# Kernel tuning notes

Measured on AMD Instinct MI355X. Metric: run time of the kernel, lower is better.

## Reference

```python
import jax, jax.numpy as jnp
import numpy as np

D_MODEL = 1024
N_HEADS = 16
D_K = D_MODEL // N_HEADS
B, S = 2, 2048


def setup_inputs() -> dict:
    key = jax.random.key(0)
    ks = jax.random.split(key, 12)
    scale = 1.0 / np.sqrt(D_MODEL)
    inp = {
        "query": jax.random.normal(ks[0], (B, S, D_MODEL), jnp.float32),
        "key": jax.random.normal(ks[1], (B, S, D_MODEL), jnp.float32),
        "value": jax.random.normal(ks[2], (B, S, D_MODEL), jnp.float32),
        "mask": jnp.tril(jnp.ones((S, S), dtype=bool))[None, None],  # (1,1,S,S) causal
        "W_q": jax.random.normal(ks[3], (D_MODEL, D_MODEL), jnp.float32) * scale,
        "b_q": jnp.zeros((D_MODEL,), jnp.float32),
        "W_k": jax.random.normal(ks[4], (D_MODEL, D_MODEL), jnp.float32) * scale,
        "b_k": jnp.zeros((D_MODEL,), jnp.float32),
        "W_v": jax.random.normal(ks[5], (D_MODEL, D_MODEL), jnp.float32) * scale,
        "b_v": jnp.zeros((D_MODEL,), jnp.float32),
        "W_o": jax.random.normal(ks[6], (D_MODEL, D_MODEL), jnp.float32) * scale,
        "b_o": jnp.zeros((D_MODEL,), jnp.float32),
    }
    return inp


def reference(query, key, value, mask, W_q, b_q, W_k, b_k, W_v, b_v, W_o, b_o):
    b = query.shape[0]
    # Linear projections (torch Linear: x @ W.T + b), split into heads -> (b,h,s,d_k)
    def proj(x, W, bias):
        y = x @ W.T + bias
        return y.reshape(b, -1, N_HEADS, D_K).transpose(0, 2, 1, 3)

    q = proj(query, W_q, b_q)
    k = proj(key, W_k, b_k)
    v = proj(value, W_v, b_v)

    # scores: (b,h,sq,sk)
    scores = jnp.einsum("bhqd,bhkd->bhqk", q, k) / jnp.sqrt(jnp.float32(D_K)).astype(q.dtype)
    scores = jnp.where(mask, scores, jnp.finfo(scores.dtype).min)
    attn = jax.nn.softmax(scores, axis=-1)
    out = jnp.einsum("bhqk,bhkd->bhqd", attn, v)  # (b,h,sq,d_k)
    out = out.transpose(0, 2, 1, 3).reshape(b, -1, D_MODEL)
    return out @ W_o.T + b_o
```

## Files before the change

kernel.cpp:

```cpp
#include <hip/hip_runtime.h>
#include <hip/hip_bf16.h>
#include <stdint.h>

#define D_MODEL 1024
#define NH 16
#define DK 64
#define BB 2
#define SS 2048
#define MROWS (BB*SS)

typedef __attribute__((ext_vector_type(8))) short bf16x8;
typedef __attribute__((ext_vector_type(4))) float f32x4;

__device__ __forceinline__ short to_bf16(float f) {
  __hip_bfloat16 h = __float2bfloat16(f);
  union { __hip_bfloat16 b; short s; } u; u.b = h; return u.s;
}

__device__ __forceinline__ f32x4 mfma16(bf16x8 a, bf16x8 b, f32x4 c) {
  return __builtin_amdgcn_mfma_f32_16x16x32_bf16(a, b, c, 0, 0, 0);
}

__device__ __forceinline__ void gload_lds16(const void* g, void* l) {
  __builtin_amdgcn_global_load_lds(
      (const __attribute__((address_space(1))) unsigned int*)g,
      (__attribute__((address_space(3))) unsigned int*)l,
      16, 0, 0);
}

__device__ __forceinline__ float max3f(float a, float b, float c) {
  return fmaxf(fmaxf(a, b), c);
}

__global__ __launch_bounds__(256) void cvt3(const float* __restrict__ a,
                                            const float* __restrict__ b,
                                            const float* __restrict__ c,
                                            short* __restrict__ oa,
                                            short* __restrict__ ob,
                                            short* __restrict__ oc) {
  const int z = blockIdx.z;
  const float* x = z == 0 ? a : z == 1 ? b : c;
  short* y = z == 0 ? oa : z == 1 ? ob : oc;
  const int i = (blockIdx.x * 256 + threadIdx.x) * 4;
  const float4 v = *(const float4*)(x + i);
  short4 o;
  o.x = to_bf16(v.x); o.y = to_bf16(v.y); o.z = to_bf16(v.z); o.w = to_bf16(v.w);
  *(short4*)(y + i) = o;
}

__global__ __launch_bounds__(256) void cvt4(const float* __restrict__ a,
                                            const float* __restrict__ b,
                                            const float* __restrict__ c,
                                            const float* __restrict__ d,
                                            short* __restrict__ oa,
                                            short* __restrict__ ob,
                                            short* __restrict__ oc,
                                            short* __restrict__ od) {
  const int z = blockIdx.z;
  const float* x = z == 0 ? a : z == 1 ? b : z == 2 ? c : d;
  short* y = z == 0 ? oa : z == 1 ? ob : z == 2 ? oc : od;
  const int i = (blockIdx.x * 256 + threadIdx.x) * 4;
  const float4 v = *(const float4*)(x + i);
  short4 o;
  o.x = to_bf16(v.x); o.y = to_bf16(v.y); o.z = to_bf16(v.z); o.w = to_bf16(v.w);
  *(short4*)(y + i) = o;
}

__global__ __launch_bounds__(256) void gemm_qkv(const short* __restrict__ Xq,
                                                const short* __restrict__ Xk,
                                                const short* __restrict__ Xv,
                                                const short* __restrict__ Wq,
                                                const short* __restrict__ Wk,
                                                const short* __restrict__ Wv,
                                                const float* __restrict__ bq,
                                                const float* __restrict__ bk,
                                                const float* __restrict__ bv,
                                                short* __restrict__ Qh,
                                                short* __restrict__ Kh,
                                                short* __restrict__ VT) {
  constexpr int K = 1024, NSTEP = K / 32;
  __shared__ __align__(16) char pool[49152];
  const int z = blockIdx.z;
  const short* A    = z == 0 ? Xq : z == 1 ? Xk : Xv;
  const short* Wt   = z == 0 ? Wq : z == 1 ? Wk : Wv;
  const float* bias = z == 0 ? bq : z == 1 ? bk : bv;

  const int tid = threadIdx.x;
  const int w = tid >> 6, lane = tid & 63;
  const int m0 = blockIdx.x * 128, n0 = blockIdx.y * 128;
  const int wm = w >> 1, wn = w & 1;
  const int fr = lane & 15, fg = lane >> 4;
  const int srow = tid >> 2, scol = (tid & 3) * 8;

  f32x4 acc[4][4] = {};

#define QKV_STAGE(buf, k0)                                                    \
  do {                                                                        \
    short* As_ = (short*)(pool + (buf) * 16384);                              \
    short* Bs_ = (short*)(pool + (buf) * 16384 + 8192);                       \
    _Pragma("unroll") for (int i = 0; i < 2; ++i) {                           \
      const int row = i * 64 + srow;                                          \
      gload_lds16(A  + (size_t)(m0 + row) * K + (k0) + scol,                  \
                  As_ + row * 32 + scol);                                     \
      gload_lds16(Wt + (size_t)(n0 + row) * K + (k0) + scol,                  \
                  Bs_ + row * 32 + scol);                                     \
    }                                                                         \
  } while (0)

  QKV_STAGE(0, 0);
  QKV_STAGE(1, 32);
  asm volatile("s_waitcnt vmcnt(4)" ::: "memory");
  __syncthreads();

  for (int t = 0; t < NSTEP; ++t) {
    if (t + 2 < NSTEP) QKV_STAGE((t + 2) % 3, (t + 2) * 32);

    const short* Ab = (const short*)(pool + (t % 3) * 16384);
    const short* Bb = (const short*)(pool + (t % 3) * 16384 + 8192);
    bf16x8 af[4], bfr[4];
#pragma unroll
    for (int i = 0; i < 4; ++i) {
      af[i]  = *(const bf16x8*)(Ab + (wm * 64 + i * 16 + fr) * 32 + fg * 8);
      bfr[i] = *(const bf16x8*)(Bb + (wn * 64 + i * 16 + fr) * 32 + fg * 8);
    }
    __builtin_amdgcn_s_setprio(1);
#pragma unroll
    for (int mi = 0; mi < 4; ++mi)
#pragma unroll
      for (int ni = 0; ni < 4; ++ni)
        acc[mi][ni] = mfma16(af[mi], bfr[ni], acc[mi][ni]);
    __builtin_amdgcn_s_setprio(0);

    if (t + 2 < NSTEP)
      asm volatile("s_waitcnt vmcnt(4)" ::: "memory");
    else
      asm volatile("s_waitcnt vmcnt(0)" ::: "memory");
    __syncthreads();
  }
#undef QKV_STAGE

  if (z < 2) {
    const float scale = (z == 0) ? 0.18033688011112042f : 1.0f;
    short* dst = (z == 0) ? Qh : Kh;
#pragma unroll
    for (int mi = 0; mi < 4; ++mi)
#pragma unroll
      for (int ni = 0; ni < 4; ++ni) {
        const int col = n0 + wn * 64 + ni * 16 + fr;
        const float bval = bias[col];
        const int h = col >> 6, d = col & 63;
#pragma unroll
        for (int r = 0; r < 4; ++r) {
          const int row = m0 + wm * 64 + mi * 16 + fg * 4 + r;
          const float val = (acc[mi][ni][r] + bval) * scale;
          const int b = row >> 11, s = row & (SS - 1);
          dst[((size_t)(b * NH + h) * SS + s) * DK + d] = to_bf16(val);
        }
      }
  } else {
    short* trs = (short*)pool;
#pragma unroll
    for (int mi = 0; mi < 4; ++mi)
#pragma unroll
      for (int ni = 0; ni < 4; ++ni) {
        const int dl = wn * 64 + ni * 16 + fr;
        const int s0 = wm * 64 + mi * 16 + fg * 4;
        const float bval = bias[n0 + dl];
        short4 sv = {to_bf16(acc[mi][ni][0] + bval), to_bf16(acc[mi][ni][1] + bval),
                     to_bf16(acc[mi][ni][2] + bval), to_bf16(acc[mi][ni][3] + bval)};
        *(short4*)(trs + dl * 128 + (s0 ^ ((dl & 7) << 3))) = sv;
      }
    __syncthreads();
    const int b = m0 >> 11, sbase = m0 & (SS - 1);
#pragma unroll
    for (int rep = 0; rep < 8; ++rep) {
      const int dl = (tid >> 4) + rep * 16;
      const int s0 = (tid & 15) * 8;
      const bf16x8 vv = *(const bf16x8*)(trs + dl * 128 + (s0 ^ ((dl & 7) << 3)));
      const int col = n0 + dl;
      const int h = col >> 6, d = col & 63;
      *(bf16x8*)(VT + ((size_t)(b * NH + h) * DK + d) * SS + sbase + s0) = vv;
    }
  }
}

__global__ __launch_bounds__(256) void gemm_out(const short* __restrict__ A,
                                                const short* __restrict__ Wt,
                                                const float* __restrict__ bias,
                                                float* __restrict__ Y) {
  constexpr int K = 1024, NSTEP = K / 32;
  __shared__ __align__(16) char pool[36864];
  const int tid = threadIdx.x;
  const int w = tid >> 6, lane = tid & 63;
  const int m0 = blockIdx.x * 128, n0 = blockIdx.y * 64;
  const int wm = w >> 1, wn = w & 1;
  const int fr = lane & 15, fg = lane >> 4;
  const int srow = tid >> 2, scol = (tid & 3) * 8;

  f32x4 acc[4][2] = {};

#define OUT_STAGE(buf, k0)                                                    \
  do {                                                                        \
    short* As_ = (short*)(pool + (buf) * 12288);                              \
    short* Bs_ = (short*)(pool + (buf) * 12288 + 8192);                       \
    _Pragma("unroll") for (int i = 0; i < 2; ++i) {                           \
      const int row = i * 64 + srow;                                          \
      gload_lds16(A + (size_t)(m0 + row) * K + (k0) + scol,                   \
                  As_ + row * 32 + scol);                                     \
    }                                                                         \
    gload_lds16(Wt + (size_t)(n0 + srow) * K + (k0) + scol,                   \
                Bs_ + srow * 32 + scol);                                      \
  } while (0)

  OUT_STAGE(0, 0);
  OUT_STAGE(1, 32);
  asm volatile("s_waitcnt vmcnt(3)" ::: "memory");
  __syncthreads();

  for (int t = 0; t < NSTEP; ++t) {
    if (t + 2 < NSTEP) OUT_STAGE((t + 2) % 3, (t + 2) * 32);

    const short* Ab = (const short*)(pool + (t % 3) * 12288);
    const short* Bb = (const short*)(pool + (t % 3) * 12288 + 8192);
    bf16x8 af[4], bfr[2];
#pragma unroll
    for (int i = 0; i < 4; ++i)
      af[i] = *(const bf16x8*)(Ab + (wm * 64 + i * 16 + fr) * 32 + fg * 8);
#pragma unroll
    for (int i = 0; i < 2; ++i)
      bfr[i] = *(const bf16x8*)(Bb + (wn * 32 + i * 16 + fr) * 32 + fg * 8);
    __builtin_amdgcn_s_setprio(1);
#pragma unroll
    for (int mi = 0; mi < 4; ++mi)
#pragma unroll
      for (int ni = 0; ni < 2; ++ni)
        acc[mi][ni] = mfma16(af[mi], bfr[ni], acc[mi][ni]);
    __builtin_amdgcn_s_setprio(0);

    if (t + 2 < NSTEP)
      asm volatile("s_waitcnt vmcnt(3)" ::: "memory");
    else
      asm volatile("s_waitcnt vmcnt(0)" ::: "memory");
    __syncthreads();
  }
#undef OUT_STAGE

#pragma unroll
  for (int mi = 0; mi < 4; ++mi)
#pragma unroll
    for (int ni = 0; ni < 2; ++ni) {
      const int col = n0 + wn * 32 + ni * 16 + fr;
      const float bval = bias[col];
#pragma unroll
      for (int r = 0; r < 4; ++r) {
        const int row = m0 + wm * 64 + mi * 16 + fg * 4 + r;
        Y[(size_t)row * D_MODEL + col] = acc[mi][ni][r] + bval;
      }
    }
}

__global__ __launch_bounds__(256) void attn_kernel(const short* __restrict__ Qh,
                                                   const short* __restrict__ Kh,
                                                   const short* __restrict__ VT,
                                                   short* __restrict__ AO) {
  __shared__ short Ks[2][2][64 * 64];
  __shared__ short Vs[2][2][64 * 64];
  __shared__ short P_lds[4][16 * 64];

  const int tid = threadIdx.x, w = tid >> 6, lane = tid & 63;
  const int fr = lane & 15, fg = lane >> 4;
  const int kr = fg * 4;
  const int swz = (fr & 7) << 4;

  const int bid = blockIdx.x;
  const int lid = ((bid & 7) << 6) | (bid >> 3);
  const int bh = lid >> 4;
  const int j = lid & 15;
  const int b = bh >> 4, h = bh & 15;

  const short* Qp = Qh + (size_t)bh * SS * DK;
  const short* Kp = Kh + (size_t)bh * SS * DK;
  const short* Vp = VT + (size_t)bh * DK * SS;

  const int sc_c = tid & 7;
  const int sc_r = tid >> 3;

  const int T0 = (j + 2) >> 1;
  const int koff0 = j * 64 - (T0 - 1) * 128;
  const int koff1 = (31 - j) * 64 - (16 - T0) * 128;

  bf16x8 qf[2];
#pragma unroll
  for (int hh = 0; hh < 2; ++hh)
    qf[hh] = *(const bf16x8*)(Qp + (size_t)(j * 64 + w * 16 + fr) * DK + hh * 32 + fg * 8);

  const short onev = (fr == 0) ? (short)0x3F80 : (short)0;
  const bf16x8 af4 = {onev, onev, onev, onev, onev, onev, onev, onev};

  f32x4 o[5] = {};
  float m_run = -1e30f;
  f32x4 stA[8], stB[8];

#define KK0(g) ((((g) < T0) ? (g) : ((g) - T0)) * 128)
#define STAGE_K(buf, kk0)                                                     \
  do {                                                                        \
    _Pragma("unroll") for (int hf = 0; hf < 2; ++hf)                          \
    _Pragma("unroll") for (int p = 0; p < 2; ++p) {                           \
      const int row = p * 32 + sc_r;                                          \
      const int sc = sc_c ^ (row & 7);                                        \
      gload_lds16(Kp + (size_t)((kk0) + hf * 64 + row) * DK + sc * 8,         \
                  &Ks[buf][hf][row * 64 + sc_c * 8]);                         \
    }                                                                         \
  } while (0)
#define STAGE_V(buf, kk0)                                                     \
  do {                                                                        \
    _Pragma("unroll") for (int hf = 0; hf < 2; ++hf)                          \
    _Pragma("unroll") for (int p = 0; p < 2; ++p) {                           \
      const int row = p * 32 + sc_r;                                          \
      const int sc = sc_c ^ (row & 7);                                        \
      gload_lds16(Vp + (size_t)row * SS + (kk0) + hf * 64 + sc * 8,           \
                  &Vs[buf][hf][row * 64 + sc_c * 8]);                         \
    }                                                                         \
  } while (0)

  auto softmax_pv = [&](int bufPrev) {
    float mm[8];
#pragma unroll
    for (int i = 0; i < 8; ++i)
      mm[i] = fmaxf(fmaxf(stB[i][0], stB[i][1]), fmaxf(stB[i][2], stB[i][3]));
    float pmax = fmaxf(max3f(mm[0], mm[1], mm[2]),
                       fmaxf(max3f(mm[3], mm[4], mm[5]), fmaxf(mm[6], mm[7])));
    pmax = fmaxf(pmax, __shfl_xor(pmax, 16));
    pmax = fmaxf(pmax, __shfl_xor(pmax, 32));

    if (!__all(pmax <= m_run + 11.0f)) {
      const float mn = fmaxf(m_run, pmax);
      const float al = __builtin_amdgcn_exp2f(m_run - mn);
      m_run = mn;
#pragma unroll
      for (int t = 0; t < 5; ++t)
#pragma unroll
        for (int r = 0; r < 4; ++r) o[t][r] *= al;
    }

#pragma unroll
    for (int hf = 0; hf < 2; ++hf) {
      char* base = (char*)P_lds[w];
#pragma unroll
      for (int kt = 0; kt < 4; ++kt) {
        short4 sv;
        sv.x = to_bf16(__builtin_amdgcn_exp2f(stB[hf * 4 + kt][0] - m_run));
        sv.y = to_bf16(__builtin_amdgcn_exp2f(stB[hf * 4 + kt][1] - m_run));
        sv.z = to_bf16(__builtin_amdgcn_exp2f(stB[hf * 4 + kt][2] - m_run));
        sv.w = to_bf16(__builtin_amdgcn_exp2f(stB[hf * 4 + kt][3] - m_run));
        *(short4*)(base + ((fr * 128 + kt * 32 + fg * 8) ^ swz)) = sv;
      }
      asm volatile("s_waitcnt lgkmcnt(0)" ::: "memory");

      const char* VsB = (const char*)Vs[bufPrev][hf];
      __builtin_amdgcn_s_setprio(1);
#pragma unroll
      for (int c = 0; c < 2; ++c) {
        const bf16x8 pf = *(const bf16x8*)((const char*)P_lds[w] +
                                           ((fr * 128 + c * 64 + fg * 16) ^ swz));
#pragma unroll
        for (int t = 0; t < 4; ++t) {
          const bf16x8 vfb = *(const bf16x8*)(VsB + (t * 16 + fr) * 128 +
                                              ((c * 64 + fg * 16) ^ swz));
          o[t] = mfma16(vfb, pf, o[t]);
        }
        o[4] = mfma16(af4, pf, o[4]);
      }
      __builtin_amdgcn_s_setprio(0);
    }
  };

  auto store_o = [&](int qbase) {
    const float l = __shfl(o[4][0], fr);
    const float inv = 1.0f / l;
    const int s = qbase + w * 16 + fr;
#pragma unroll
    for (int t = 0; t < 4; ++t) {
      short4 ov = {to_bf16(o[t][0] * inv), to_bf16(o[t][1] * inv),
                   to_bf16(o[t][2] * inv), to_bf16(o[t][3] * inv)};
      *(short4*)(AO + (size_t)(b * SS + s) * D_MODEL + h * 64 + t * 16 + kr) = ov;
    }
  };

  STAGE_K(0, 0);
  STAGE_V(0, 0);
  asm volatile("s_waitcnt vmcnt(0)" ::: "memory");
  __syncthreads();

  for (int g = 0; g < 17; ++g) {
    if (g == T0) {
#pragma unroll
      for (int hh = 0; hh < 2; ++hh)
        qf[hh] = *(const bf16x8*)(Qp + (size_t)((31 - j) * 64 + w * 16 + fr) * DK + hh * 32 + fg * 8);
    }

    if (g + 1 < 17) STAGE_K((g + 1) & 1, KK0(g + 1));

    {
      __builtin_amdgcn_s_setprio(1);
#pragma unroll
      for (int hf = 0; hf < 2; ++hf) {
        const char* KsB = (const char*)Ks[g & 1][hf];
#pragma unroll
        for (int kt = 0; kt < 4; ++kt) {
          const bf16x8 k0f = *(const bf16x8*)(KsB + (kt * 16 + fr) * 128 + ((fg * 16) ^ swz));
          const bf16x8 k1f = *(const bf16x8*)(KsB + (kt * 16 + fr) * 128 + ((64 + fg * 16) ^ swz));
          f32x4 zz = {};
          zz = mfma16(k0f, qf[0], zz);
          zz = mfma16(k1f, qf[1], zz);
          stA[hf * 4 + kt] = zz;
        }
      }
      __builtin_amdgcn_s_setprio(0);
    }
    if (g == T0 - 1 || g == 16) {
      const int koff = (g == 16) ? koff1 : koff0;
#pragma unroll
      for (int hf = 0; hf < 2; ++hf)
#pragma unroll
        for (int kt = 0; kt < 4; ++kt)
#pragma unroll
          for (int r = 0; r < 4; ++r)
            if (hf * 64 + kt * 16 + kr + r > koff + w * 16 + fr)
              stA[hf * 4 + kt][r] = -1e30f;
    }

    if (g > 0) {
      softmax_pv((g - 1) & 1);
      if (g == T0) {
        store_o(j * 64);
#pragma unroll
        for (int t = 0; t < 5; ++t)
#pragma unroll
          for (int r = 0; r < 4; ++r) o[t][r] = 0.f;
        m_run = -1e30f;
      }
    }

#pragma unroll
    for (int i = 0; i < 8; ++i) stB[i] = stA[i];

    __syncthreads();
    if (g + 1 < 17) {
      STAGE_V((g + 1) & 1, KK0(g + 1));
      asm volatile("s_waitcnt vmcnt(4)" ::: "memory");
    } else {
      asm volatile("s_waitcnt vmcnt(0)" ::: "memory");
    }
  }

  softmax_pv(16 & 1);
  store_o((31 - j) * 64);
#undef STAGE_K
#undef STAGE_V
#undef KK0
}

extern "C" void kernel_launch(void* const* d_in, const int* in_sizes, int n_in,
                              void* d_out, int out_size, void* d_ws, size_t ws_size,
                              hipStream_t stream) {
  const float* q  = (const float*)d_in[0];
  const float* k  = (const float*)d_in[1];
  const float* v  = (const float*)d_in[2];
  const float* Wq = (const float*)d_in[4];
  const float* bq = (const float*)d_in[5];
  const float* Wk = (const float*)d_in[6];
  const float* bk = (const float*)d_in[7];
  const float* Wv = (const float*)d_in[8];
  const float* bv = (const float*)d_in[9];
  const float* Wo = (const float*)d_in[10];
  const float* bo = (const float*)d_in[11];

  char* ws = (char*)d_ws;
  const size_t MB = 1u << 20;
  short* Xq = (short*)(ws + 0 * MB);
  short* Xk = (short*)(ws + 8 * MB);
  short* Xv = (short*)(ws + 16 * MB);
  short* Bq = (short*)(ws + 24 * MB);
  short* Bk = (short*)(ws + 26 * MB);
  short* Bv = (short*)(ws + 28 * MB);
  short* Bo = (short*)(ws + 30 * MB);
  short* Qh = (short*)(ws + 32 * MB);
  short* Kh = (short*)(ws + 40 * MB);
  short* VT = (short*)(ws + 48 * MB);
  short* AO = (short*)(ws + 56 * MB);

  cvt3<<<dim3(MROWS * D_MODEL / 1024, 1, 3), 256, 0, stream>>>(q, k, v, Xq, Xk, Xv);
  cvt4<<<dim3(D_MODEL * D_MODEL / 1024, 1, 4), 256, 0, stream>>>(Wq, Wk, Wv, Wo, Bq, Bk, Bv, Bo);

  gemm_qkv<<<dim3(MROWS / 128, D_MODEL / 128, 3), 256, 0, stream>>>(
      Xq, Xk, Xv, Bq, Bk, Bv, bq, bk, bv, Qh, Kh, VT);

  attn_kernel<<<dim3(512), 256, 0, stream>>>(Qh, Kh, VT, AO);

  gemm_out<<<dim3(MROWS / 128, D_MODEL / 64), 256, 0, stream>>>(AO, Bo, bo, (float*)d_out);
}
```

Baseline: 120.1 us.

## Double attention query tile to 128 rows per block and merge conversion kernels

Each attention workgroup now processes 128 query rows, with each wave owning two 16-row query tiles. Every K/V fragment loaded from LDS is reused across both tiles, and the grid shrinks from 512 to 256 blocks with launch bounds set for one block per CU. The causal pairing scheme moves to 8 chunks of 128 rows. The two fp32-to-bf16 conversion kernels are merged into one launch, with a bounds check for the smaller weight tensors. The trade-off is higher register pressure from doubled accumulators and score tiles, and fewer blocks to fill the 256 CUs.

```diff
diff --git a/kernel.cpp b/kernel.cpp
--- a/kernel.cpp
+++ b/kernel.cpp
@@ -32,34 +32,33 @@
   return fmaxf(fmaxf(a, b), c);
 }
 
-__global__ __launch_bounds__(256) void cvt3(const float* __restrict__ a,
-                                            const float* __restrict__ b,
-                                            const float* __restrict__ c,
-                                            short* __restrict__ oa,
-                                            short* __restrict__ ob,
-                                            short* __restrict__ oc) {
+__global__ __launch_bounds__(256) void cvt7(const float* __restrict__ x0,
+                                            const float* __restrict__ x1,
+                                            const float* __restrict__ x2,
+                                            const float* __restrict__ w0,
+                                            const float* __restrict__ w1,
+                                            const float* __restrict__ w2,
+                                            const float* __restrict__ w3,
+                                            short* __restrict__ y0,
+                                            short* __restrict__ y1,
+                                            short* __restrict__ y2,
+                                            short* __restrict__ y3,
+                                            short* __restrict__ y4,
+                                            short* __restrict__ y5,
+                                            short* __restrict__ y6) {
   const int z = blockIdx.z;
-  const float* x = z == 0 ? a : z == 1 ? b : c;
-  short* y = z == 0 ? oa : z == 1 ? ob : oc;
+  const float* x; short* y; int n;
+  switch (z) {
+    case 0: x = x0; y = y0; n = MROWS * D_MODEL; break;
+    case 1: x = x1; y = y1; n = MROWS * D_MODEL; break;
+    case 2: x = x2; y = y2; n = MROWS * D_MODEL; break;
+    case 3: x = w0; y = y3; n = D_MODEL * D_MODEL; break;
+    case 4: x = w1; y = y4; n = D_MODEL * D_MODEL; break;
+    case 5: x = w2; y = y5; n = D_MODEL * D_MODEL; break;
+    default: x = w3; y = y6; n = D_MODEL * D_MODEL; break;
+  }
   const int i = (blockIdx.x * 256 + threadIdx.x) * 4;
-  const float4 v = *(const float4*)(x + i);
-  short4 o;
-  o.x = to_bf16(v.x); o.y = to_bf16(v.y); o.z = to_bf16(v.z); o.w = to_bf16(v.w);
-  *(short4*)(y + i) = o;
-}
-
-__global__ __launch_bounds__(256) void cvt4(const float* __restrict__ a,
-                                            const float* __restrict__ b,
-                                            const float* __restrict__ c,
-                                            const float* __restrict__ d,
-                                            short* __restrict__ oa,
-                                            short* __restrict__ ob,
-                                            short* __restrict__ oc,
-                                            short* __restrict__ od) {
-  const int z = blockIdx.z;
-  const float* x = z == 0 ? a : z == 1 ? b : z == 2 ? c : d;
-  short* y = z == 0 ? oa : z == 1 ? ob : z == 2 ? oc : od;
-  const int i = (blockIdx.x * 256 + threadIdx.x) * 4;
+  if (i >= n) return;
   const float4 v = *(const float4*)(x + i);
   short4 o;
   o.x = to_bf16(v.x); o.y = to_bf16(v.y); o.z = to_bf16(v.z); o.w = to_bf16(v.w);
@@ -259,13 +258,13 @@
     }
 }
 
-__global__ __launch_bounds__(256) void attn_kernel(const short* __restrict__ Qh,
-                                                   const short* __restrict__ Kh,
-                                                   const short* __restrict__ VT,
-                                                   short* __restrict__ AO) {
-  __shared__ short Ks[2][2][64 * 64];
-  __shared__ short Vs[2][2][64 * 64];
-  __shared__ short P_lds[4][16 * 64];
+__global__ __launch_bounds__(256, 1) void attn_kernel(const short* __restrict__ Qh,
+                                                      const short* __restrict__ Kh,
+                                                      const short* __restrict__ VT,
+                                                      short* __restrict__ AO) {
+  __shared__ short Ks[2][128 * 64];
+  __shared__ short Vs[2][64 * 128];
+  __shared__ short P_lds[4][2][16 * 64];
 
   const int tid = threadIdx.x, w = tid >> 6, lane = tid & 63;
   const int fr = lane & 15, fg = lane >> 4;
@@ -273,117 +272,144 @@
   const int swz = (fr & 7) << 4;
 
   const int bid = blockIdx.x;
-  const int lid = ((bid & 7) << 6) | (bid >> 3);
-  const int bh = lid >> 4;
-  const int j = lid & 15;
+  const int lid = ((bid & 7) << 5) | (bid >> 3);
+  const int bh = lid >> 3;
+  const int j = lid & 7;
   const int b = bh >> 4, h = bh & 15;
 
   const short* Qp = Qh + (size_t)bh * SS * DK;
   const short* Kp = Kh + (size_t)bh * SS * DK;
   const short* Vp = VT + (size_t)bh * DK * SS;
 
-  const int sc_c = tid & 7;
-  const int sc_r = tid >> 3;
-
-  const int T0 = (j + 2) >> 1;
-  const int koff0 = j * 64 - (T0 - 1) * 128;
-  const int koff1 = (31 - j) * 64 - (16 - T0) * 128;
-
-  bf16x8 qf[2];
-#pragma unroll
-  for (int hh = 0; hh < 2; ++hh)
-    qf[hh] = *(const bf16x8*)(Qp + (size_t)(j * 64 + w * 16 + fr) * DK + hh * 32 + fg * 8);
+  const int kc = tid & 7,  kvr = tid >> 3;
+  const int vc = tid & 15, vvr = tid >> 4;
+
+  const int C0 = j + 1;
+  const int qb0 = j * 128, qb1 = (15 - j) * 128;
+
+  bf16x8 qf[2][2];
+#pragma unroll
+  for (int qt = 0; qt < 2; ++qt)
+#pragma unroll
+    for (int hh = 0; hh < 2; ++hh)
+      qf[qt][hh] = *(const bf16x8*)(Qp + (size_t)(qb0 + w * 32 + qt * 16 + fr) * DK + hh * 32 + fg * 8);
 
   const short onev = (fr == 0) ? (short)0x3F80 : (short)0;
   const bf16x8 af4 = {onev, onev, onev, onev, onev, onev, onev, onev};
 
-  f32x4 o[5] = {};
-  float m_run = -1e30f;
-  f32x4 stA[8], stB[8];
-
-#define KK0(g) ((((g) < T0) ? (g) : ((g) - T0)) * 128)
+  f32x4 o[5][2] = {};
+  float m_run[2] = {-1e30f, -1e30f};
+  f32x4 stA[2][8], stB[2][8];
+
+#define KK0(g) ((((g) < C0) ? (g) : ((g) - C0)) * 128)
 #define STAGE_K(buf, kk0)                                                     \
   do {                                                                        \
-    _Pragma("unroll") for (int hf = 0; hf < 2; ++hf)                          \
-    _Pragma("unroll") for (int p = 0; p < 2; ++p) {                           \
-      const int row = p * 32 + sc_r;                                          \
-      const int sc = sc_c ^ (row & 7);                                        \
-      gload_lds16(Kp + (size_t)((kk0) + hf * 64 + row) * DK + sc * 8,         \
-                  &Ks[buf][hf][row * 64 + sc_c * 8]);                         \
+    _Pragma("unroll") for (int p = 0; p < 4; ++p) {                           \
+      const int row = p * 32 + kvr;                                           \
+      const int sc = kc ^ (row & 7);                                          \
+      gload_lds16(Kp + (size_t)((kk0) + row) * DK + sc * 8,                   \
+                  &Ks[buf][row * 64 + kc * 8]);                               \
     }                                                                         \
   } while (0)
 #define STAGE_V(buf, kk0)                                                     \
   do {                                                                        \
-    _Pragma("unroll") for (int hf = 0; hf < 2; ++hf)                          \
-    _Pragma("unroll") for (int p = 0; p < 2; ++p) {                           \
-      const int row = p * 32 + sc_r;                                          \
-      const int sc = sc_c ^ (row & 7);                                        \
-      gload_lds16(Vp + (size_t)row * SS + (kk0) + hf * 64 + sc * 8,           \
-                  &Vs[buf][hf][row * 64 + sc_c * 8]);                         \
+    _Pragma("unroll") for (int p = 0; p < 4; ++p) {                           \
+      const int row = p * 16 + vvr;                                           \
+      const int sc = vc ^ (row & 7);                                          \
+      gload_lds16(Vp + (size_t)row * SS + (kk0) + sc * 8,                     \
+                  &Vs[buf][row * 128 + vc * 8]);                              \
     }                                                                         \
   } while (0)
 
   auto softmax_pv = [&](int bufPrev) {
-    float mm[8];
-#pragma unroll
-    for (int i = 0; i < 8; ++i)
-      mm[i] = fmaxf(fmaxf(stB[i][0], stB[i][1]), fmaxf(stB[i][2], stB[i][3]));
-    float pmax = fmaxf(max3f(mm[0], mm[1], mm[2]),
+    float pmax[2];
+#pragma unroll
+    for (int qt = 0; qt < 2; ++qt) {
+      float mm[8];
+#pragma unroll
+      for (int i = 0; i < 8; ++i)
+        mm[i] = fmaxf(fmaxf(stB[qt][i][0], stB[qt][i][1]),
+                      fmaxf(stB[qt][i][2], stB[qt][i][3]));
+      float pm = fmaxf(max3f(mm[0], mm[1], mm[2]),
                        fmaxf(max3f(mm[3], mm[4], mm[5]), fmaxf(mm[6], mm[7])));
-    pmax = fmaxf(pmax, __shfl_xor(pmax, 16));
-    pmax = fmaxf(pmax, __shfl_xor(pmax, 32));
-
-    if (!__all(pmax <= m_run + 11.0f)) {
-      const float mn = fmaxf(m_run, pmax);
-      const float al = __builtin_amdgcn_exp2f(m_run - mn);
-      m_run = mn;
-#pragma unroll
-      for (int t = 0; t < 5; ++t)
-#pragma unroll
-        for (int r = 0; r < 4; ++r) o[t][r] *= al;
+      pm = fmaxf(pm, __shfl_xor(pm, 16));
+      pm = fmaxf(pm, __shfl_xor(pm, 32));
+      pmax[qt] = pm;
+    }
+
+    const bool ok = (pmax[0] <= m_run[0] + 11.0f) && (pmax[1] <= m_run[1] + 11.0f);
+    if (!__all(ok)) {
+#pragma unroll
+      for (int qt = 0; qt < 2; ++qt) {
+        const float mn = fmaxf(m_run[qt], pmax[qt]);
+        const float al = __builtin_amdgcn_exp2f(m_run[qt] - mn);
+        m_run[qt] = mn;
+#pragma unroll
+        for (int t = 0; t < 5; ++t)
+#pragma unroll
+          for (int r = 0; r < 4; ++r) o[t][qt][r] *= al;
+      }
     }
 
 #pragma unroll
     for (int hf = 0; hf < 2; ++hf) {
-      char* base = (char*)P_lds[w];
-#pragma unroll
-      for (int kt = 0; kt < 4; ++kt) {
-        short4 sv;
-        sv.x = to_bf16(__builtin_amdgcn_exp2f(stB[hf * 4 + kt][0] - m_run));
-        sv.y = to_bf16(__builtin_amdgcn_exp2f(stB[hf * 4 + kt][1] - m_run));
-        sv.z = to_bf16(__builtin_amdgcn_exp2f(stB[hf * 4 + kt][2] - m_run));
-        sv.w = to_bf16(__builtin_amdgcn_exp2f(stB[hf * 4 + kt][3] - m_run));
-        *(short4*)(base + ((fr * 128 + kt * 32 + fg * 8) ^ swz)) = sv;
-      }
+#pragma unroll
+      for (int qt = 0; qt < 2; ++qt) {
+        char* base = (char*)P_lds[w][qt];
+#pragma unroll
+        for (int kt = 0; kt < 4; ++kt) {
+          const int kk = hf * 4 + kt;
+          short4 sv;
+          sv.x = to_bf16(__builtin_amdgcn_exp2f(stB[qt][kk][0] - m_run[qt]));
+          sv.y = to_bf16(__builtin_amdgcn_exp2f(stB[qt][kk][1] - m_run[qt]));
+          sv.z = to_bf16(__builtin_amdgcn_exp2f(stB[qt][kk][2] - m_run[qt]));
+          sv.w = to_bf16(__builtin_amdgcn_exp2f(stB[qt][kk][3] - m_run[qt]));
+          *(short4*)(base + ((fr * 128 + kt * 32 + fg * 8) ^ swz)) = sv;
+        }
+      }
+      const char* VsB = (const char*)Vs[bufPrev];
+      bf16x8 vfh[2][4];
+#pragma unroll
+      for (int c = 0; c < 2; ++c)
+#pragma unroll
+        for (int t = 0; t < 4; ++t)
+          vfh[c][t] = *(const bf16x8*)(VsB + (t * 16 + fr) * 256 +
+                                       ((hf * 128 + c * 64 + fg * 16) ^ swz));
       asm volatile("s_waitcnt lgkmcnt(0)" ::: "memory");
 
-      const char* VsB = (const char*)Vs[bufPrev][hf];
       __builtin_amdgcn_s_setprio(1);
 #pragma unroll
       for (int c = 0; c < 2; ++c) {
-        const bf16x8 pf = *(const bf16x8*)((const char*)P_lds[w] +
-                                           ((fr * 128 + c * 64 + fg * 16) ^ swz));
-#pragma unroll
-        for (int t = 0; t < 4; ++t) {
-          const bf16x8 vfb = *(const bf16x8*)(VsB + (t * 16 + fr) * 128 +
-                                              ((c * 64 + fg * 16) ^ swz));
-          o[t] = mfma16(vfb, pf, o[t]);
-        }
-        o[4] = mfma16(af4, pf, o[4]);
+        bf16x8 pf[2];
+#pragma unroll
+        for (int qt = 0; qt < 2; ++qt)
+          pf[qt] = *(const bf16x8*)((const char*)P_lds[w][qt] +
+                                    ((fr * 128 + c * 64 + fg * 16) ^ swz));
+#pragma unroll
+        for (int t = 0; t < 4; ++t)
+#pragma unroll
+          for (int qt = 0; qt < 2; ++qt)
+            o[t][qt] = mfma16(vfh[c][t], pf[qt], o[t][qt]);
+#pragma unroll
+        for (int qt = 0; qt < 2; ++qt)
+          o[4][qt] = mfma16(af4, pf[qt], o[4][qt]);
       }
       __builtin_amdgcn_s_setprio(0);
     }
   };
 
   auto store_o = [&](int qbase) {
-    const float l = __shfl(o[4][0], fr);
-    const float inv = 1.0f / l;
-    const int s = qbase + w * 16 + fr;
-#pragma unroll
-    for (int t = 0; t < 4; ++t) {
-      short4 ov = {to_bf16(o[t][0] * inv), to_bf16(o[t][1] * inv),
-                   to_bf16(o[t][2] * inv), to_bf16(o[t][3] * inv)};
-      *(short4*)(AO + (size_t)(b * SS + s) * D_MODEL + h * 64 + t * 16 + kr) = ov;
+#pragma unroll
+    for (int qt = 0; qt < 2; ++qt) {
+      const float l = __shfl(o[4][qt][0], fr);
+      const float inv = 1.0f / l;
+      const int s = qbase + w * 32 + qt * 16 + fr;
+#pragma unroll
+      for (int t = 0; t < 4; ++t) {
+        short4 ov = {to_bf16(o[t][qt][0] * inv), to_bf16(o[t][qt][1] * inv),
+                     to_bf16(o[t][qt][2] * inv), to_bf16(o[t][qt][3] * inv)};
+        *(short4*)(AO + (size_t)(b * SS + s) * D_MODEL + h * 64 + t * 16 + kr) = ov;
+      }
     }
   };
 
@@ -393,57 +419,61 @@
   __syncthreads();
 
   for (int g = 0; g < 17; ++g) {
-    if (g == T0) {
-#pragma unroll
-      for (int hh = 0; hh < 2; ++hh)
-        qf[hh] = *(const bf16x8*)(Qp + (size_t)((31 - j) * 64 + w * 16 + fr) * DK + hh * 32 + fg * 8);
+    if (g == C0) {
+#pragma unroll
+      for (int qt = 0; qt < 2; ++qt)
+#pragma unroll
+        for (int hh = 0; hh < 2; ++hh)
+          qf[qt][hh] = *(const bf16x8*)(Qp + (size_t)(qb1 + w * 32 + qt * 16 + fr) * DK + hh * 32 + fg * 8);
     }
 
     if (g + 1 < 17) STAGE_K((g + 1) & 1, KK0(g + 1));
 
     {
+      const char* KsB = (const char*)Ks[g & 1];
       __builtin_amdgcn_s_setprio(1);
 #pragma unroll
-      for (int hf = 0; hf < 2; ++hf) {
-        const char* KsB = (const char*)Ks[g & 1][hf];
-#pragma unroll
-        for (int kt = 0; kt < 4; ++kt) {
-          const bf16x8 k0f = *(const bf16x8*)(KsB + (kt * 16 + fr) * 128 + ((fg * 16) ^ swz));
-          const bf16x8 k1f = *(const bf16x8*)(KsB + (kt * 16 + fr) * 128 + ((64 + fg * 16) ^ swz));
+      for (int kt = 0; kt < 8; ++kt) {
+        const bf16x8 k0f = *(const bf16x8*)(KsB + (kt * 16 + fr) * 128 + ((fg * 16) ^ swz));
+        const bf16x8 k1f = *(const bf16x8*)(KsB + (kt * 16 + fr) * 128 + ((64 + fg * 16) ^ swz));
+#pragma unroll
+        for (int qt = 0; qt < 2; ++qt) {
           f32x4 zz = {};
-          zz = mfma16(k0f, qf[0], zz);
-          zz = mfma16(k1f, qf[1], zz);
-          stA[hf * 4 + kt] = zz;
+          zz = mfma16(k0f, qf[qt][0], zz);
+          zz = mfma16(k1f, qf[qt][1], zz);
+          stA[qt][kt] = zz;
         }
       }
       __builtin_amdgcn_s_setprio(0);
     }
-    if (g == T0 - 1 || g == 16) {
-      const int koff = (g == 16) ? koff1 : koff0;
-#pragma unroll
-      for (int hf = 0; hf < 2; ++hf)
-#pragma unroll
-        for (int kt = 0; kt < 4; ++kt)
+    if (g == C0 - 1 || g == 16) {
+#pragma unroll
+      for (int qt = 0; qt < 2; ++qt)
+#pragma unroll
+        for (int kt = 0; kt < 8; ++kt)
 #pragma unroll
           for (int r = 0; r < 4; ++r)
-            if (hf * 64 + kt * 16 + kr + r > koff + w * 16 + fr)
-              stA[hf * 4 + kt][r] = -1e30f;
+            if (kt * 16 + kr + r > w * 32 + qt * 16 + fr) stA[qt][kt][r] = -1e30f;
     }
 
     if (g > 0) {
       softmax_pv((g - 1) & 1);
-      if (g == T0) {
-        store_o(j * 64);
+      if (g == C0) {
+        store_o(qb0);
 #pragma unroll
         for (int t = 0; t < 5; ++t)
 #pragma unroll
-          for (int r = 0; r < 4; ++r) o[t][r] = 0.f;
-        m_run = -1e30f;
-      }
-    }
-
-#pragma unroll
-    for (int i = 0; i < 8; ++i) stB[i] = stA[i];
+          for (int qt = 0; qt < 2; ++qt)
+#pragma unroll
+            for (int r = 0; r < 4; ++r) o[t][qt][r] = 0.f;
+        m_run[0] = -1e30f; m_run[1] = -1e30f;
+      }
+    }
+
+#pragma unroll
+    for (int qt = 0; qt < 2; ++qt)
+#pragma unroll
+      for (int i = 0; i < 8; ++i) stB[qt][i] = stA[qt][i];
 
     __syncthreads();
     if (g + 1 < 17) {
@@ -455,7 +485,7 @@
   }
 
   softmax_pv(16 & 1);
-  store_o((31 - j) * 64);
+  store_o(qb1);
 #undef STAGE_K
 #undef STAGE_V
 #undef KK0
@@ -490,13 +520,13 @@
   short* VT = (short*)(ws + 48 * MB);
   short* AO = (short*)(ws + 56 * MB);
 
-  cvt3<<<dim3(MROWS * D_MODEL / 1024, 1, 3), 256, 0, stream>>>(q, k, v, Xq, Xk, Xv);
-  cvt4<<<dim3(D_MODEL * D_MODEL / 1024, 1, 4), 256, 0, stream>>>(Wq, Wk, Wv, Wo, Bq, Bk, Bv, Bo);
+  cvt7<<<dim3(MROWS * D_MODEL / 1024, 1, 7), 256, 0, stream>>>(
+      q, k, v, Wq, Wk, Wv, Wo, Xq, Xk, Xv, Bq, Bk, Bv, Bo);
 
   gemm_qkv<<<dim3(MROWS / 128, D_MODEL / 128, 3), 256, 0, stream>>>(
       Xq, Xk, Xv, Bq, Bk, Bv, bq, bk, bv, Qh, Kh, VT);
 
-  attn_kernel<<<dim3(512), 256, 0, stream>>>(Qh, Kh, VT, AO);
+  attn_kernel<<<dim3(256), 256, 0, stream>>>(Qh, Kh, VT, AO);
 
   gemm_out<<<dim3(MROWS / 128, D_MODEL / 64), 256, 0, stream>>>(AO, Bo, bo, (float*)d_out);
 }
```

Result: slower. 128.3 us (+6.9%).
